# Kernel optimization log

Measured on AMD Instinct MI355X. Metric: run time of the kernel, lower is better.

## Reference

```python
import jax, jax.numpy as jnp
import numpy as np

S, T, B = 128, 64, 64          # src_len, trg_len, batch
E, H, D, A, V = 512, 512, 1024, 256, 32000  # emb, enc_hid, dec_hid(=2H), attn, vocab
PAD = 0


def _p(key, shape, scale=0.02):
    return jax.random.normal(key, shape, dtype=jnp.float32) * scale


def setup_inputs() -> dict:
    key = jax.random.key(0)
    ks = jax.random.split(key, 20)
    return {
        'src': jax.random.randint(ks[0], (S, B), 0, V, dtype=jnp.int32),
        'trg': jax.random.randint(ks[1], (T, B), 0, V, dtype=jnp.int32),
        'enc_emb': _p(ks[2], (V, E)),
        'Wf_ih': _p(ks[3], (4 * H, E)), 'Wf_hh': _p(ks[4], (4 * H, H)), 'bf': jnp.zeros((4 * H,), jnp.float32),
        'Wb_ih': _p(ks[5], (4 * H, E)), 'Wb_hh': _p(ks[6], (4 * H, H)), 'bb': jnp.zeros((4 * H,), jnp.float32),
        'Wa': _p(ks[7], (A, 2 * H + D)), 'ba': jnp.zeros((A,), jnp.float32),
        'v': _p(ks[8], (A,)),
        'dec_emb': _p(ks[9], (V, E)),
        'Wd_ih': _p(ks[10], (4 * D, E + 2 * H)), 'Wd_hh': _p(ks[11], (4 * D, D)), 'bd': jnp.zeros((4 * D,), jnp.float32),
        'Wo': _p(ks[12], (V, 2 * H + D + E)), 'bo': jnp.zeros((V,), jnp.float32),
    }


def lstm_cell(x, h, c, W_ih, W_hh, b):
    # PyTorch gate order: i, f, g, o
    g = x @ W_ih.T + h @ W_hh.T + b
    i, f, gg, o = jnp.split(g, 4, axis=-1)
    c2 = jax.nn.sigmoid(f) * c + jax.nn.sigmoid(i) * jnp.tanh(gg)
    h2 = jax.nn.sigmoid(o) * jnp.tanh(c2)
    return h2, c2


def seq2seq_fwd(src, trg, enc_emb, Wf_ih, Wf_hh, bf, Wb_ih, Wb_hh, bb,
                Wa, ba, v, dec_emb, Wd_ih, Wd_hh, bd, Wo, bo):
    emb = enc_emb[src]                                   # [S,B,E]
    z = jnp.zeros((B, H), emb.dtype)

    def fstep(carry, x):
        h, c = lstm_cell(x, *carry, Wf_ih, Wf_hh, bf)
        return (h, c), h

    def bstep(carry, x):
        h, c = lstm_cell(x, *carry, Wb_ih, Wb_hh, bb)
        return (h, c), h

    (hf, cf), hs_f = jax.lax.scan(fstep, (z, z), emb)
    (hb, cb), hs_b = jax.lax.scan(bstep, (z, z), emb[::-1])
    enc_out = jnp.concatenate([hs_f, hs_b[::-1]], axis=-1)   # [S,B,2H]

    h0 = jnp.concatenate([hf, hb], axis=-1)              # [B,D]
    c0 = jnp.concatenate([cf, cb], axis=-1)

    mask = (src != PAD).T                                # [B,S]
    enc_bse = enc_out.transpose(1, 0, 2)                 # [B,S,2H]

    def dstep(carry, tok):
        h, c = carry
        emb_t = dec_emb[tok]                             # [B,E]
        hrep = jnp.broadcast_to(h[:, None, :], (B, S, D))
        energy = jnp.tanh(jnp.concatenate([hrep, enc_bse], -1) @ Wa.T + ba)  # [B,S,A]
        scores = energy @ v                              # [B,S]
        scores = jnp.where(mask, scores, jnp.float32(-1e10))
        a = jax.nn.softmax(scores, axis=1)
        ctx = jnp.einsum('bs,bse->be', a, enc_bse)       # [B,2H]
        x = jnp.concatenate([emb_t, ctx], axis=-1)
        h2, c2 = lstm_cell(x, h, c, Wd_ih, Wd_hh, bd)
        pred = jnp.concatenate([h2, ctx, emb_t], -1) @ Wo.T + bo  # [B,V]
        return (h2, c2), pred

    # teacher_forcing_ratio = 1.0 -> input at step t is trg[t-1]
    _, preds = jax.lax.scan(dstep, (h0, c0), trg[:-1])
    outputs = jnp.concatenate([jnp.zeros((1, B, V), preds.dtype), preds], axis=0)
    return outputs                                       # [T,B,V]


def reference(src, trg, enc_emb, Wf_ih, Wf_hh, bf, Wb_ih, Wb_hh, bb,
              Wa, ba, v, dec_emb, Wd_ih, Wd_hh, bd, Wo, bo):
    return seq2seq_fwd(src, trg, enc_emb, Wf_ih, Wf_hh, bf, Wb_ih, Wb_hh, bb,
                       Wa, ba, v, dec_emb, Wd_ih, Wd_hh, bd, Wo, bo)
```

## Files before the change

kernel.cpp:

```cpp
#include <hip/hip_runtime.h>

#define SLEN  128
#define BATCH 64
#define EMB   512
#define HID   512
#define DDEC  1024
#define ATT   256
#define VOC   32000
#define TSTEPS 63
#define SLOT  1024

typedef _Float16 f16x4 __attribute__((ext_vector_type(4)));
typedef _Float16 f16x8 __attribute__((ext_vector_type(8)));
typedef float    f32x4 __attribute__((ext_vector_type(4)));

union HQ  { unsigned long long q[2]; f16x8 v; };
union HP  { _Float16 h[2]; unsigned u; };
union HP4 { _Float16 h[4]; f16x4 v4; unsigned long long u; };

__device__ __forceinline__ float sigmoidf_(float x) { return 1.0f / (1.0f + __expf(-x)); }
__device__ __forceinline__ float tanhf_(float x)    { return 1.0f - 2.0f / (__expf(2.0f * x) + 1.0f); }

__device__ __forceinline__ void st_u32(void* p, unsigned v) {
    __hip_atomic_store((unsigned*)p, v, __ATOMIC_RELAXED, __HIP_MEMORY_SCOPE_AGENT);
}
__device__ __forceinline__ void st_u64(void* p, unsigned long long v) {
    __hip_atomic_store((unsigned long long*)p, v, __ATOMIC_RELAXED, __HIP_MEMORY_SCOPE_AGENT);
}
__device__ __forceinline__ unsigned long long ld_u64(const void* p) {
    return __hip_atomic_load((const unsigned long long*)p, __ATOMIC_RELAXED, __HIP_MEMORY_SCOPE_AGENT);
}
__device__ __forceinline__ void st_i32(int* p, int v) {
    __hip_atomic_store(p, v, __ATOMIC_RELAXED, __HIP_MEMORY_SCOPE_AGENT);
}
__device__ __forceinline__ int ld_i32(const int* p) {
    return __hip_atomic_load(p, __ATOMIC_RELAXED, __HIP_MEMORY_SCOPE_AGENT);
}

__device__ __forceinline__ void barf(int* flags, int* gen, int narr, int myid,
                                     int epoch, bool amDet) {
    __syncthreads();
    if (amDet) {
        if (threadIdx.x == 0 && myid < narr) st_i32(flags + myid * SLOT, epoch);
        if ((int)threadIdx.x < narr) {
            while (ld_i32(flags + threadIdx.x * SLOT) < epoch)
                __builtin_amdgcn_s_sleep(2);
        }
        __syncthreads();
        if (threadIdx.x == 0) st_i32(gen, epoch);
    } else {
        if (threadIdx.x == 0) {
            if (myid < narr) st_i32(flags + myid * SLOT, epoch);
            while (ld_i32(gen) < epoch)
                __builtin_amdgcn_s_sleep(4);
        }
    }
    __syncthreads();
}

__global__ __launch_bounds__(256) void init_convert(
    const int* __restrict__ src, const int* __restrict__ trg,
    const float* __restrict__ enc_emb, const float* __restrict__ dec_emb,
    const float* __restrict__ Wf_ih, const float* __restrict__ Wf_hh,
    const float* __restrict__ Wb_ih, const float* __restrict__ Wb_hh,
    const float* __restrict__ Wa, const float* __restrict__ Wd_ih, const float* __restrict__ Wd_hh,
    float* __restrict__ out0,
    _Float16* __restrict__ Wenc16, _Float16* __restrict__ Wd16, _Float16* __restrict__ Wa16,
    _Float16* __restrict__ emb_src16, _Float16* __restrict__ predA,
    float* __restrict__ c_enc, _Float16* __restrict__ h16_enc, int* __restrict__ bar_ws)
{
    long idx = (long)blockIdx.x * 256 + threadIdx.x;
    if (idx < 2048000L) { out0[idx] = 0.f; return; }
    idx -= 2048000L;
    if (idx < 4194304L) {
        int dir = (int)(idx >> 21);
        int rem = (int)(idx & ((1 << 21) - 1));
        int rr = rem >> 10, c = rem & 1023;
        int d = rr >> 2, qg = rr & 3;
        const float* Wih = dir ? Wb_ih : Wf_ih;
        const float* Whh = dir ? Wb_hh : Wf_hh;
        float v = (c < 512) ? Wih[(long)(qg * 512 + d) * 512 + c]
                            : Whh[(long)(qg * 512 + d) * 512 + (c - 512)];
        Wenc16[idx] = (_Float16)v; return;
    }
    idx -= 4194304L;
    if (idx < 10485760L) {
        int rr = (int)(idx / 2560), c = (int)(idx % 2560);
        int d = rr >> 2, qg = rr & 3;
        float v = (c < 1536) ? Wd_ih[(long)(qg * 1024 + d) * 1536 + c]
                             : Wd_hh[(long)(qg * 1024 + d) * 1024 + (c - 1536)];
        Wd16[idx] = (_Float16)v; return;
    }
    idx -= 10485760L;
    if (idx < 262144L) {
        int rr = (int)(idx >> 10), c = (int)(idx & 1023);
        Wa16[idx] = (_Float16)Wa[(long)rr * 2048 + c]; return;
    }
    idx -= 262144L;
    if (idx < 4194304L) {
        int sb = (int)(idx >> 9), e = (int)(idx & 511);
        int tok = src[sb];
        emb_src16[idx] = (_Float16)enc_emb[(long)tok * 512 + e]; return;
    }
    idx -= 4194304L;
    if (idx < 2064384L) {
        int rI = (int)(idx >> 9), e = (int)(idx & 511);
        int tok = trg[rI];
        predA[(long)(64 + rI) * 2560 + 2048 + e] = (_Float16)dec_emb[(long)tok * 512 + e]; return;
    }
    idx -= 2064384L;
    if (idx < 65536L) { c_enc[idx] = 0.f; return; }
    idx -= 65536L;
    if (idx < 65536L) { h16_enc[idx] = (_Float16)0.f; return; }
    idx -= 65536L;
    if (idx < 527360L) { bar_ws[idx] = 0; }
}

__global__ __launch_bounds__(256, 1) void enc_coop(
    const _Float16* __restrict__ Wenc16, const _Float16* __restrict__ emb_src16,
    _Float16* __restrict__ h16_enc, float* __restrict__ c_enc,
    const float* __restrict__ bf, const float* __restrict__ bb,
    _Float16* __restrict__ enc_out16, int* __restrict__ bar_ws)
{
    __shared__ _Float16 Wl[16384];
    __shared__ float gbuf[16][65];

    const int t = threadIdx.x, lane = t & 63, w = t >> 6;
    const int blk = blockIdx.x, dir = blk >> 7, tile = blk & 127;
    const int r16 = lane & 15, kg = lane >> 4;
    int* gflags = bar_ws + (257 + dir * 129) * SLOT;
    int* ggen   = gflags + 128 * SLOT;
    const bool amDet = (tile == 127);

    #pragma unroll
    for (int i = 0; i < 8; ++i) {
        int h0 = (i * 256 + t) * 8;
        int kc = h0 >> 9, l = (h0 >> 3) & 63;
        f16x8 v = *(const f16x8*)(Wenc16 + ((size_t)(dir * 2048 + tile * 16 + (l & 15))) * 1024 + (l >> 4) * 8 + kc * 32);
        *(f16x8*)&Wl[h0] = v;
    }

    const float* bias = dir ? bb : bf;
    const int pb = t & 63, pp = (t >> 6) & 1;
    float bias2[2][4];
    float creg2[2] = {0.f, 0.f};
    if (t < 128) {
        #pragma unroll
        for (int j = 0; j < 2; ++j)
            #pragma unroll
            for (int q = 0; q < 4; ++q)
                bias2[j][q] = bias[q * 512 + tile * 4 + pp * 2 + j];
    }
    __syncthreads();

    for (int s = 0; s < SLEN; ++s) {
        const int par = s & 1;
        const int s_eff = dir ? (127 - s) : s;
        const _Float16* Ax = emb_src16 + ((size_t)(s_eff * 64 + w * 16 + r16)) * 512 + kg * 8;
        const unsigned long long* Hq =
            (const unsigned long long*)(h16_enc + ((size_t)((par * 2 + dir) * 64 + w * 16 + r16)) * 512);
        f32x4 a0 = {}, a1 = {};
        #pragma unroll 8
        for (int kc = 0; kc < 16; ++kc) {
            f16x8 bx = *(const f16x8*)&Wl[kc * 512 + lane * 8];
            f16x8 ax = *(const f16x8*)(Ax + kc * 32);
            a0 = __builtin_amdgcn_mfma_f32_16x16x32_f16(ax, bx, a0, 0, 0, 0);
            f16x8 bh = *(const f16x8*)&Wl[(16 + kc) * 512 + lane * 8];
            HQ hq;
            hq.q[0] = ld_u64(Hq + kc * 8 + kg * 2);
            hq.q[1] = ld_u64(Hq + kc * 8 + kg * 2 + 1);
            a1 = __builtin_amdgcn_mfma_f32_16x16x32_f16(hq.v, bh, a1, 0, 0, 0);
        }
        #pragma unroll
        for (int rI = 0; rI < 4; ++rI)
            gbuf[r16][w * 16 + kg * 4 + rI] = a0[rI] + a1[rI];
        __syncthreads();
        if (t < 128) {
            HP hp;
            #pragma unroll
            for (int j = 0; j < 2; ++j) {
                const int dl = pp * 2 + j;
                float g0 = gbuf[dl * 4 + 0][pb] + bias2[j][0];
                float g1 = gbuf[dl * 4 + 1][pb] + bias2[j][1];
                float g2 = gbuf[dl * 4 + 2][pb] + bias2[j][2];
                float g3 = gbuf[dl * 4 + 3][pb] + bias2[j][3];
                float c2 = sigmoidf_(g1) * creg2[j] + sigmoidf_(g0) * tanhf_(g2);
                float h2 = sigmoidf_(g3) * tanhf_(c2);
                creg2[j] = c2;
                hp.h[j] = (_Float16)h2;
            }
            const int d0 = tile * 4 + pp * 2;
            st_u32((void*)(h16_enc + ((size_t)((par ^ 1) * 2 + dir) * 64 + pb) * 512 + d0), hp.u);
            *(unsigned*)(enc_out16 + ((size_t)s_eff * 64 + pb) * 1024 + dir * 512 + d0) = hp.u;
        }
        barf(gflags, ggen, 128, tile, s + 1, amDet);
    }
    if (t < 128) {
        const int d0 = tile * 4 + pp * 2;
        c_enc[((size_t)dir * 64 + pb) * 512 + d0] = creg2[0];
        c_enc[((size_t)dir * 64 + pb) * 512 + d0 + 1] = creg2[1];
    }
}

__global__ __launch_bounds__(256, 1) void dec_coop(
    const _Float16* __restrict__ Wd16, const _Float16* __restrict__ Wa16,
    const float* __restrict__ bd, const float* __restrict__ vvec,
    const int* __restrict__ src, const _Float16* __restrict__ enc_part16,
    const _Float16* __restrict__ enc_out16, const float* __restrict__ c_enc,
    _Float16* __restrict__ predA, int* __restrict__ bar_ws)
{
    __shared__ _Float16 Wl[40960];
    __shared__ float gbuf[16][65];
    __shared__ float ha[256], sv[256], sc[128], red[128];

    const int t = threadIdx.x, lane = t & 63, w = t >> 6;
    const int tile = blockIdx.x;
    const int r16 = lane & 15, kg = lane >> 4;
    int* gflags = bar_ws;
    int* ggen   = gflags + 256 * SLOT;
    const bool amDet = (tile == 255);

    #pragma unroll
    for (int i = 0; i < 20; ++i) {
        int h0 = (i * 256 + t) * 8;
        int kc = h0 >> 9, l = (h0 >> 3) & 63;
        f16x8 v = *(const f16x8*)(Wd16 + ((size_t)(tile * 16 + (l & 15))) * 2560 + (l >> 4) * 8 + kc * 32);
        *(f16x8*)&Wl[h0] = v;
    }

    const int pb = t & 63, pp = (t >> 6) & 1;
    float bias2[2][4], creg2[2] = {0.f, 0.f};
    if (t < 128) {
        #pragma unroll
        for (int j = 0; j < 2; ++j) {
            const int dg = tile * 4 + pp * 2 + j;
            #pragma unroll
            for (int q = 0; q < 4; ++q) bias2[j][q] = bd[q * 1024 + dg];
            creg2[j] = (dg < 512) ? c_enc[(size_t)pb * 512 + dg]
                                  : c_enc[(size_t)(64 + pb) * 512 + (dg - 512)];
        }
    }

    const int b0 = blockIdx.x;
    if (b0 < 64) {
        sv[t] = vvec[t];
        #pragma unroll
        for (int i = 0; i < 2; ++i) {
            int pidx = i * 256 + t;
            int d = pidx * 2;
            const size_t rbase = (d < 512) ? (size_t)(127 * 64 + b0) * 1024 : (size_t)(0 * 64 + b0) * 1024;
            HP hp;
            hp.h[0] = enc_out16[rbase + d];
            hp.h[1] = enc_out16[rbase + d + 1];
            st_u32((void*)(predA + (size_t)b0 * 2560 + d), hp.u);
        }
    }
    barf(gflags, ggen, 64, tile, 1, amDet);

    for (int tt = 0; tt < TSTEPS; ++tt) {
        if (b0 < 64) {
            const int base_m = b0 & 48;
            const _Float16* Ahh = predA + ((size_t)(tt * 64 + base_m + r16)) * 2560 + kg * 8;
            f32x4 acc4[4] = {};
            #pragma unroll 4
            for (int kc = 0; kc < 32; ++kc) {
                f16x8 a = *(const f16x8*)(Ahh + kc * 32);
                #pragma unroll
                for (int jj = 0; jj < 4; ++jj) {
                    f16x8 bw = *(const f16x8*)(Wa16 + ((size_t)((w * 4 + jj) * 16 + r16)) * 1024 + kg * 8 + kc * 32);
                    acc4[jj] = __builtin_amdgcn_mfma_f32_16x16x32_f16(a, bw, acc4[jj], 0, 0, 0);
                }
            }
            if (kg == ((b0 & 15) >> 2)) {
                #pragma unroll
                for (int jj = 0; jj < 4; ++jj)
                    ha[(w * 4 + jj) * 16 + r16] = acc4[jj][b0 & 3];
            }
            __syncthreads();
            if (t < 128) {
                const f16x8* ep = (const f16x8*)(enc_part16 + ((size_t)t * 64 + b0) * 256);
                float acc = 0.f;
                #pragma unroll 4
                for (int j8 = 0; j8 < 32; ++j8) {
                    f16x8 e = ep[j8];
                    #pragma unroll
                    for (int u = 0; u < 8; ++u)
                        acc += tanhf_(ha[j8 * 8 + u] + (float)e[u]) * sv[j8 * 8 + u];
                }
                float scv = (src[t * 64 + b0] != 0) ? acc : -1e10f;
                sc[t] = scv; red[t] = scv;
            }
            __syncthreads();
            for (int off = 64; off > 0; off >>= 1) { if (t < off) red[t] = fmaxf(red[t], red[t + off]); __syncthreads(); }
            const float mx = red[0];
            __syncthreads();
            if (t < 128) { float e = __expf(sc[t] - mx); sc[t] = e; red[t] = e; }
            __syncthreads();
            for (int off = 64; off > 0; off >>= 1) { if (t < off) red[t] += red[t + off]; __syncthreads(); }
            const float inv = 1.0f / red[0];
            __syncthreads();
            float a0 = 0.f, a1 = 0.f, a2 = 0.f, a3 = 0.f;
            for (int sI = 0; sI < 128; ++sI) {
                float as = sc[sI] * inv;
                f16x4 ev = *(const f16x4*)(enc_out16 + ((size_t)sI * 64 + b0) * 1024 + t * 4);
                a0 += as * (float)ev[0]; a1 += as * (float)ev[1];
                a2 += as * (float)ev[2]; a3 += as * (float)ev[3];
            }
            HP4 o;
            o.h[0] = (_Float16)a0; o.h[1] = (_Float16)a1;
            o.h[2] = (_Float16)a2; o.h[3] = (_Float16)a3;
            st_u64((void*)(predA + ((size_t)(64 + tt * 64 + b0)) * 2560 + 1024 + t * 4), o.u);
        }
        barf(gflags, ggen, 64, tile, 2 * tt + 2, amDet);
        {
            const _Float16* Ae = predA + ((size_t)(64 + tt * 64 + w * 16 + r16)) * 2560 + kg * 8;
            const _Float16* Ah = predA + ((size_t)(tt * 64 + w * 16 + r16)) * 2560 + kg * 8;
            f32x4 ae = {}, ac = {}, ah = {};
            #pragma unroll 8
            for (int kc = 0; kc < 16; ++kc) {
                f16x8 bw = *(const f16x8*)&Wl[kc * 512 + lane * 8];
                f16x8 a = *(const f16x8*)(Ae + 2048 + kc * 32);
                ae = __builtin_amdgcn_mfma_f32_16x16x32_f16(a, bw, ae, 0, 0, 0);
            }
            #pragma unroll 8
            for (int kc = 0; kc < 32; ++kc) {
                f16x8 bw = *(const f16x8*)&Wl[(16 + kc) * 512 + lane * 8];
                f16x8 a = *(const f16x8*)(Ae + 1024 + kc * 32);
                ac = __builtin_amdgcn_mfma_f32_16x16x32_f16(a, bw, ac, 0, 0, 0);
            }
            #pragma unroll 8
            for (int kc = 0; kc < 32; ++kc) {
                f16x8 bw = *(const f16x8*)&Wl[(48 + kc) * 512 + lane * 8];
                f16x8 a = *(const f16x8*)(Ah + kc * 32);
                ah = __builtin_amdgcn_mfma_f32_16x16x32_f16(a, bw, ah, 0, 0, 0);
            }
            #pragma unroll
            for (int rI = 0; rI < 4; ++rI)
                gbuf[r16][w * 16 + kg * 4 + rI] = ae[rI] + ac[rI] + ah[rI];
            __syncthreads();
            if (t < 128) {
                HP hp;
                #pragma unroll
                for (int j = 0; j < 2; ++j) {
                    const int dl = pp * 2 + j;
                    float g0 = gbuf[dl * 4 + 0][pb] + bias2[j][0];
                    float g1 = gbuf[dl * 4 + 1][pb] + bias2[j][1];
                    float g2 = gbuf[dl * 4 + 2][pb] + bias2[j][2];
                    float g3 = gbuf[dl * 4 + 3][pb] + bias2[j][3];
                    float c2 = sigmoidf_(g1) * creg2[j] + sigmoidf_(g0) * tanhf_(g2);
                    float h2 = sigmoidf_(g3) * tanhf_(c2);
                    creg2[j] = c2;
                    hp.h[j] = (_Float16)h2;
                }
                st_u32((void*)(predA + ((size_t)(64 + tt * 64 + pb)) * 2560 + tile * 4 + pp * 2), hp.u);
            }
        }
        barf(gflags, ggen, 256, tile, 2 * tt + 3, amDet);
    }
}

__global__ __launch_bounds__(64) void enc_step_mfma(
    const _Float16* __restrict__ Wenc16, const _Float16* __restrict__ emb_src16,
    _Float16* __restrict__ h16_enc, float* __restrict__ c_enc,
    const float* __restrict__ bf, const float* __restrict__ bb,
    _Float16* __restrict__ enc_out16, int s)
{
    __shared__ float gbuf[16 * 66];
    const int lane = threadIdx.x;
    const int blk = blockIdx.x;
    const int dir = blk >> 7, tile = blk & 127;
    const int par = s & 1;
    const int s_eff = dir ? (SLEN - 1 - s) : s;
    const int r16 = lane & 15, kg = lane >> 4;

    const _Float16* Bw = Wenc16 + ((size_t)(dir * 2048 + tile * 16 + r16)) * 1024 + kg * 8;
    const _Float16* Ax = emb_src16 + ((size_t)(s_eff * 64 + r16)) * 512 + kg * 8;
    const _Float16* Ah = h16_enc + ((size_t)((par * 2 + dir) * 64 + r16)) * 512 + kg * 8;

    f32x4 acc[4] = {};
    #pragma unroll 4
    for (int kc = 0; kc < 16; ++kc) {
        f16x8 bfr = *(const f16x8*)(Bw + kc * 32);
        #pragma unroll
        for (int m = 0; m < 4; ++m) {
            f16x8 a = *(const f16x8*)(Ax + kc * 32 + (size_t)m * 16 * 512);
            acc[m] = __builtin_amdgcn_mfma_f32_16x16x32_f16(a, bfr, acc[m], 0, 0, 0);
        }
    }
    #pragma unroll 4
    for (int kc = 0; kc < 16; ++kc) {
        f16x8 bfr = *(const f16x8*)(Bw + 512 + kc * 32);
        #pragma unroll
        for (int m = 0; m < 4; ++m) {
            f16x8 a = *(const f16x8*)(Ah + kc * 32 + (size_t)m * 16 * 512);
            acc[m] = __builtin_amdgcn_mfma_f32_16x16x32_f16(a, bfr, acc[m], 0, 0, 0);
        }
    }
    #pragma unroll
    for (int m = 0; m < 4; ++m)
        #pragma unroll
        for (int rI = 0; rI < 4; ++rI)
            gbuf[r16 * 66 + m * 16 + kg * 4 + rI] = acc[m][rI];
    __syncthreads();

    const float* bias = dir ? bb : bf;
    const int b = lane;
    #pragma unroll
    for (int dl = 0; dl < 4; ++dl) {
        const int d = tile * 4 + dl;
        float g0 = gbuf[(dl * 4 + 0) * 66 + b] + bias[d];
        float g1 = gbuf[(dl * 4 + 1) * 66 + b] + bias[512 + d];
        float g2 = gbuf[(dl * 4 + 2) * 66 + b] + bias[1024 + d];
        float g3 = gbuf[(dl * 4 + 3) * 66 + b] + bias[1536 + d];
        const size_t cur = ((size_t)(par * 2 + dir) * 64 + b) * 512 + d;
        const size_t nxt = ((size_t)((par ^ 1) * 2 + dir) * 64 + b) * 512 + d;
        float c2 = sigmoidf_(g1) * c_enc[cur] + sigmoidf_(g0) * tanhf_(g2);
        float h2 = sigmoidf_(g3) * tanhf_(c2);
        c_enc[nxt] = c2;
        h16_enc[nxt] = (_Float16)h2;
        enc_out16[((size_t)s_eff * 64 + b) * 1024 + dir * 512 + d] = (_Float16)h2;
    }
}

__global__ __launch_bounds__(256) void dec_init(
    const _Float16* __restrict__ enc_out16, const float* __restrict__ c_enc,
    _Float16* __restrict__ predA, float* __restrict__ c_dec)
{
    int idx = blockIdx.x * 256 + threadIdx.x;
    int b = (idx >> 10) & 63, d = idx & 1023;
    if (idx < 65536) {
        _Float16 v = (d < 512) ? enc_out16[(size_t)(127 * 64 + b) * 1024 + d]
                               : enc_out16[(size_t)(0 * 64 + b) * 1024 + d];
        predA[(size_t)b * 2560 + d] = v;
    } else {
        float v = (d < 512) ? c_enc[((size_t)(0 * 2 + 0) * 64 + b) * 512 + d]
                            : c_enc[((size_t)(0 * 2 + 1) * 64 + b) * 512 + (d - 512)];
        c_dec[(size_t)b * 1024 + d] = v;
    }
}

__global__ __launch_bounds__(64) void hatt_mfma(
    const _Float16* __restrict__ predA, const _Float16* __restrict__ Wa16,
    float* __restrict__ hatt, int t)
{
    const int lane = threadIdx.x;
    const int tile = blockIdx.x;
    const int r16 = lane & 15, kg = lane >> 4;
    const _Float16* Ap = predA + ((size_t)(t * 64 + r16)) * 2560 + kg * 8;
    const _Float16* Bw = Wa16 + ((size_t)(tile * 16 + r16)) * 1024 + kg * 8;
    f32x4 acc[4] = {};
    #pragma unroll 4
    for (int kc = 0; kc < 32; ++kc) {
        f16x8 bfr = *(const f16x8*)(Bw + kc * 32);
        #pragma unroll
        for (int m = 0; m < 4; ++m) {
            f16x8 a = *(const f16x8*)(Ap + kc * 32 + (size_t)m * 16 * 2560);
            acc[m] = __builtin_amdgcn_mfma_f32_16x16x32_f16(a, bfr, acc[m], 0, 0, 0);
        }
    }
    #pragma unroll
    for (int m = 0; m < 4; ++m)
        #pragma unroll
        for (int rI = 0; rI < 4; ++rI)
            hatt[(size_t)(m * 16 + kg * 4 + rI) * 256 + tile * 16 + r16] = acc[m][rI];
}

__global__ __launch_bounds__(256) void attn_step(
    const int* __restrict__ src, const float* __restrict__ hatt, const float* __restrict__ vvec,
    const _Float16* __restrict__ enc_part16, const _Float16* __restrict__ enc_out16,
    _Float16* __restrict__ predA, int t)
{
    __shared__ float ha[256], sv[256], sc[128], red[128];
    const int b = blockIdx.x, tid = threadIdx.x;
    ha[tid] = hatt[b * 256 + tid];
    sv[tid] = vvec[tid];
    __syncthreads();
    if (tid < 128) {
        const f16x8* ep = (const f16x8*)(enc_part16 + ((size_t)tid * 64 + b) * 256);
        float acc = 0.f;
        #pragma unroll 4
        for (int j8 = 0; j8 < 32; ++j8) {
            f16x8 e = ep[j8];
            #pragma unroll
            for (int u = 0; u < 8; ++u)
                acc += tanhf_(ha[j8 * 8 + u] + (float)e[u]) * sv[j8 * 8 + u];
        }
        float scv = (src[tid * 64 + b] != 0) ? acc : -1e10f;
        sc[tid] = scv; red[tid] = scv;
    }
    __syncthreads();
    for (int off = 64; off > 0; off >>= 1) { if (tid < off) red[tid] = fmaxf(red[tid], red[tid + off]); __syncthreads(); }
    const float mx = red[0];
    __syncthreads();
    if (tid < 128) { float e = __expf(sc[tid] - mx); sc[tid] = e; red[tid] = e; }
    __syncthreads();
    for (int off = 64; off > 0; off >>= 1) { if (tid < off) red[tid] += red[tid + off]; __syncthreads(); }
    const float inv = 1.0f / red[0];
    __syncthreads();

    float a0 = 0.f, a1 = 0.f, a2 = 0.f, a3 = 0.f;
    for (int sI = 0; sI < 128; ++sI) {
        float as = sc[sI] * inv;
        f16x4 ev = *(const f16x4*)(enc_out16 + ((size_t)sI * 64 + b) * 1024 + tid * 4);
        a0 += as * (float)ev[0]; a1 += as * (float)ev[1];
        a2 += as * (float)ev[2]; a3 += as * (float)ev[3];
    }
    f16x4 o = { (_Float16)a0, (_Float16)a1, (_Float16)a2, (_Float16)a3 };
    *(f16x4*)(predA + ((size_t)(64 + t * 64 + b)) * 2560 + 1024 + tid * 4) = o;
}

__global__ __launch_bounds__(64) void dec_gates(
    const _Float16* __restrict__ Wd16, const float* __restrict__ bd,
    float* __restrict__ c_dec, _Float16* __restrict__ predA, int t)
{
    __shared__ float gbuf[16 * 66];
    const int lane = threadIdx.x;
    const int tile = blockIdx.x;
    const int par = t & 1;
    const int r16 = lane & 15, kg = lane >> 4;
    const _Float16* Bw = Wd16 + ((size_t)(tile * 16 + r16)) * 2560 + kg * 8;
    const _Float16* At = predA + ((size_t)(64 + t * 64 + r16)) * 2560 + kg * 8;
    const _Float16* Ah = predA + ((size_t)(t * 64 + r16)) * 2560 + kg * 8;
    f32x4 acc[4] = {};
    #pragma unroll 4
    for (int kc = 0; kc < 16; ++kc) {
        f16x8 bfr = *(const f16x8*)(Bw + kc * 32);
        #pragma unroll
        for (int m = 0; m < 4; ++m) {
            f16x8 a = *(const f16x8*)(At + 2048 + kc * 32 + (size_t)m * 16 * 2560);
            acc[m] = __builtin_amdgcn_mfma_f32_16x16x32_f16(a, bfr, acc[m], 0, 0, 0);
        }
    }
    #pragma unroll 4
    for (int kc = 0; kc < 32; ++kc) {
        f16x8 bfr = *(const f16x8*)(Bw + 512 + kc * 32);
        #pragma unroll
        for (int m = 0; m < 4; ++m) {
            f16x8 a = *(const f16x8*)(At + 1024 + kc * 32 + (size_t)m * 16 * 2560);
            acc[m] = __builtin_amdgcn_mfma_f32_16x16x32_f16(a, bfr, acc[m], 0, 0, 0);
        }
    }
    #pragma unroll 4
    for (int kc = 0; kc < 32; ++kc) {
        f16x8 bfr = *(const f16x8*)(Bw + 1536 + kc * 32);
        #pragma unroll
        for (int m = 0; m < 4; ++m) {
            f16x8 a = *(const f16x8*)(Ah + kc * 32 + (size_t)m * 16 * 2560);
            acc[m] = __builtin_amdgcn_mfma_f32_16x16x32_f16(a, bfr, acc[m], 0, 0, 0);
        }
    }
    #pragma unroll
    for (int m = 0; m < 4; ++m)
        #pragma unroll
        for (int rI = 0; rI < 4; ++rI)
            gbuf[r16 * 66 + m * 16 + kg * 4 + rI] = acc[m][rI];
    __syncthreads();

    const int b = lane;
    #pragma unroll
    for (int dl = 0; dl < 4; ++dl) {
        const int d = tile * 4 + dl;
        float g0 = gbuf[(dl * 4 + 0) * 66 + b] + bd[d];
        float g1 = gbuf[(dl * 4 + 1) * 66 + b] + bd[1024 + d];
        float g2 = gbuf[(dl * 4 + 2) * 66 + b] + bd[2048 + d];
        float g3 = gbuf[(dl * 4 + 3) * 66 + b] + bd[3072 + d];
        float c2 = sigmoidf_(g1) * c_dec[(size_t)(par * 64 + b) * 1024 + d] + sigmoidf_(g0) * tanhf_(g2);
        float h2 = sigmoidf_(g3) * tanhf_(c2);
        c_dec[(size_t)((par ^ 1) * 64 + b) * 1024 + d] = c2;
        predA[((size_t)(64 + t * 64 + b)) * 2560 + d] = (_Float16)h2;
    }
}

__global__ __launch_bounds__(256, 2) void gemm_a16(
    const _Float16* __restrict__ A, int lda,
    const float* __restrict__ B, int ldb,
    const float* __restrict__ bias,
    void* __restrict__ Cv, int ldc, int K, int Mvalid, int ntn, int c16)
{
    __shared__ _Float16 As[8192];
    __shared__ _Float16 Bs[8192];

    const int nwg = gridDim.x;
    const int id = blockIdx.x;
    const int q = nwg >> 3, r = nwg & 7;
    const int xcd = id & 7, ix = id >> 3;
    const int wg = (xcd < r) ? (xcd * (q + 1) + ix) : (r * (q + 1) + (xcd - r) * q + ix);
    const int per = ntn << 3;
    const int g = wg / per, rem = wg % per;
    const int mt = g * 8 + (rem & 7), nt = rem >> 3;

    const int t = threadIdx.x, lane = t & 63, wid = t >> 6;
    const int wr = wid >> 1, wc = wid & 1;

    const int arow_s = t >> 3, ac8 = t & 7;
    const int brow_s = t >> 4, bc4 = t & 15;
    const _Float16* Ap = A + (size_t)(mt * 128 + arow_s) * lda + ac8 * 8;
    const float*    Bp = B + (size_t)(nt * 128 + brow_s) * ldb + bc4 * 4;
    const int awx = (ac8 * 8) ^ ((arow_s & 7) << 3);
    const int bwx = (bc4 * 4) ^ ((brow_s & 7) << 3);

    const int kts = K >> 6;
    f32x4 acc[4][4] = {};
    f16x8 ra[4]; float4 rb[8];
    #pragma unroll
    for (int i = 0; i < 4; ++i) ra[i] = *(const f16x8*)(Ap + (size_t)i * 32 * lda);
    #pragma unroll
    for (int i = 0; i < 8; ++i) rb[i] = *(const float4*)(Bp + (size_t)i * 16 * ldb);

    const int abase = (wr * 64 + (lane & 15)) * 64 + (lane >> 4) * 8;
    const int bbase = (wc * 64 + (lane & 15)) * 64 + (lane >> 4) * 8;
    const int sxor = (lane & 7) << 3;

    for (int kt = 0; kt < kts; ++kt) {
        f16x4 cb[8];
        #pragma unroll
        for (int i = 0; i < 8; ++i)
            cb[i] = (f16x4){(_Float16)rb[i].x, (_Float16)rb[i].y, (_Float16)rb[i].z, (_Float16)rb[i].w};
        __syncthreads();
        #pragma unroll
        for (int i = 0; i < 4; ++i)
            *(f16x8*)&As[(arow_s + i * 32) * 64 + awx] = ra[i];
        #pragma unroll
        for (int i = 0; i < 8; ++i)
            *(f16x4*)&Bs[(brow_s + i * 16) * 64 + bwx] = cb[i];
        __syncthreads();
        if (kt + 1 < kts) {
            #pragma unroll
            for (int i = 0; i < 4; ++i) ra[i] = *(const f16x8*)(Ap + (size_t)i * 32 * lda + (kt + 1) * 64);
            #pragma unroll
            for (int i = 0; i < 8; ++i) rb[i] = *(const float4*)(Bp + (size_t)i * 16 * ldb + (kt + 1) * 64);
        }
        #pragma unroll
        for (int kk = 0; kk < 2; ++kk) {
            f16x8 af[4], bfr[4];
            #pragma unroll
            for (int m = 0; m < 4; ++m) af[m]  = *(const f16x8*)&As[(abase + m * 16 * 64 + kk * 32) ^ sxor];
            #pragma unroll
            for (int n = 0; n < 4; ++n) bfr[n] = *(const f16x8*)&Bs[(bbase + n * 16 * 64 + kk * 32) ^ sxor];
            #pragma unroll
            for (int m = 0; m < 4; ++m)
                #pragma unroll
                for (int n = 0; n < 4; ++n)
                    acc[m][n] = __builtin_amdgcn_mfma_f32_16x16x32_f16(af[m], bfr[n], acc[m][n], 0, 0, 0);
        }
    }

    const int ccol = nt * 128 + wc * 64 + (lane & 15);
    const int crow0 = mt * 128 + wr * 64 + ((lane >> 4) << 2);
    float bv[4];
    #pragma unroll
    for (int n = 0; n < 4; ++n) bv[n] = bias[ccol + n * 16];
    #pragma unroll
    for (int m = 0; m < 4; ++m) {
        #pragma unroll
        for (int rI = 0; rI < 4; ++rI) {
            const int row = crow0 + m * 16 + rI;
            if (row < Mvalid) {
                if (c16) {
                    _Float16* C = (_Float16*)Cv;
                    #pragma unroll
                    for (int n = 0; n < 4; ++n)
                        C[(size_t)row * ldc + ccol + n * 16] = (_Float16)(acc[m][n][rI] + bv[n]);
                } else {
                    float* C = (float*)Cv;
                    #pragma unroll
                    for (int n = 0; n < 4; ++n)
                        C[(size_t)row * ldc + ccol + n * 16] = acc[m][n][rI] + bv[n];
                }
            }
        }
    }
}

extern "C" void kernel_launch(void* const* d_in, const int* in_sizes, int n_in,
                              void* d_out, int out_size, void* d_ws, size_t ws_size,
                              hipStream_t stream) {
    const int*   src     = (const int*)d_in[0];
    const int*   trg     = (const int*)d_in[1];
    const float* enc_emb = (const float*)d_in[2];
    const float* Wf_ih   = (const float*)d_in[3];
    const float* Wf_hh   = (const float*)d_in[4];
    const float* bf      = (const float*)d_in[5];
    const float* Wb_ih   = (const float*)d_in[6];
    const float* Wb_hh   = (const float*)d_in[7];
    const float* bb      = (const float*)d_in[8];
    const float* Wa      = (const float*)d_in[9];
    const float* ba      = (const float*)d_in[10];
    const float* vvec    = (const float*)d_in[11];
    const float* dec_emb = (const float*)d_in[12];
    const float* Wd_ih   = (const float*)d_in[13];
    const float* Wd_hh   = (const float*)d_in[14];
    const float* bd      = (const float*)d_in[15];
    const float* Wo      = (const float*)d_in[16];
    const float* bo      = (const float*)d_in[17];
    float* out = (float*)d_out;

    char* w = (char*)d_ws;
    _Float16* Wenc16     = (_Float16*)(w);
    _Float16* Wd16       = (_Float16*)(w + 8388608);
    _Float16* Wa16       = (_Float16*)(w + 29360128);
    _Float16* emb_src16  = (_Float16*)(w + 29884416);
    _Float16* enc_out16  = (_Float16*)(w + 38273024);
    _Float16* predA      = (_Float16*)(w + 55050240);
    _Float16* h16_enc    = (_Float16*)(w + 76349440);
    float*    c_enc      = (float*)   (w + 76611584);
    float*    c_dec      = (float*)   (w + 77135872);
    float*    hatt       = (float*)   (w + 77660160);
    _Float16* enc_part16 = (_Float16*)(w + 77725696);
    int*      bar_ws     = (int*)     (w + 81920000);
    const size_t need_bytes = 84029440;
    if (ws_size < need_bytes) return;

    init_convert<<<93428, 256, 0, stream>>>(
        src, trg, enc_emb, dec_emb, Wf_ih, Wf_hh, Wb_ih, Wb_hh, Wa, Wd_ih, Wd_hh,
        out, Wenc16, Wd16, Wa16, emb_src16, predA, c_enc, h16_enc, bar_ws);

    {
        const _Float16* a0 = Wenc16; const _Float16* a1 = emb_src16;
        _Float16* a2 = h16_enc; float* a3 = c_enc;
        const float* a4 = bf; const float* a5 = bb;
        _Float16* a6 = enc_out16; int* a7 = bar_ws;
        void* args[] = { &a0, &a1, &a2, &a3, &a4, &a5, &a6, &a7 };
        hipError_t e = hipLaunchCooperativeKernel((const void*)enc_coop, dim3(256), dim3(256), args, 0, stream);
        if (e != hipSuccess) {
            for (int s = 0; s < SLEN; ++s)
                enc_step_mfma<<<256, 64, 0, stream>>>(Wenc16, emb_src16, h16_enc, c_enc, bf, bb, enc_out16, s);
        }
    }

    gemm_a16<<<128, 256, 0, stream>>>(enc_out16, 1024, Wa + 1024, 2048, ba,
                                      enc_part16, 256, 1024, 8192, 2, 1);

    {
        const _Float16* a0 = Wd16; const _Float16* a1 = Wa16;
        const float* a2 = bd; const float* a3 = vvec;
        const int* a4 = src; const _Float16* a5 = enc_part16;
        const _Float16* a6 = enc_out16; const float* a7 = c_enc;
        _Float16* a8 = predA; int* a9 = bar_ws;
        void* args[] = { &a0, &a1, &a2, &a3, &a4, &a5, &a6, &a7, &a8, &a9 };
        hipError_t e = hipLaunchCooperativeKernel((const void*)dec_coop, dim3(256), dim3(256), args, 0, stream);
        if (e != hipSuccess) {
            dec_init<<<512, 256, 0, stream>>>(enc_out16, c_enc, predA, c_dec);
            for (int t = 0; t < TSTEPS; ++t) {
                hatt_mfma<<<16, 64, 0, stream>>>(predA, Wa16, hatt, t);
                attn_step<<<64, 256, 0, stream>>>(src, hatt, vvec, enc_part16, enc_out16, predA, t);
                dec_gates<<<256, 64, 0, stream>>>(Wd16, bd, c_dec, predA, t);
            }
        }
    }

    gemm_a16<<<8000, 256, 0, stream>>>(predA + (size_t)64 * 2560, 2560, Wo, 2560, bo,
                                       out + (size_t)64 * VOC, VOC, 2560, 4032, 250, 0);
}
```

Measured before the change: 5.999 ms.

## Repartition encoder and decoder cooperative kernels across fewer blocks with LDS-staged activations

The encoder now splits work into four groups (direction × batch half) of 64 blocks, each handling 32 hidden units for 32 batch rows. It stages the input embedding and hidden state in swizzled LDS and holds a larger weight tile in LDS. The decoder drops from 256 to 64 blocks of 512 threads, so every block computes attention and the gate GEMM while streaming Wd from global memory instead of LDS. Grid barriers now span only 64 participants, which reduces sync cost, but each block carries more per-step work and the decoder loses its LDS-resident weights.

Result: slower. 6.867 ms (+14.5%).

```diff
diff --git a/kernel.cpp b/kernel.cpp
--- a/kernel.cpp
+++ b/kernel.cpp
@@ -113,7 +113,7 @@
     idx -= 65536L;
     if (idx < 65536L) { h16_enc[idx] = (_Float16)0.f; return; }
     idx -= 65536L;
-    if (idx < 527360L) { bar_ws[idx] = 0; }
+    if (idx < 332800L) { bar_ws[idx] = 0; }
 }
 
 __global__ __launch_bounds__(256, 1) void enc_coop(
@@ -122,64 +122,85 @@
     const float* __restrict__ bf, const float* __restrict__ bb,
     _Float16* __restrict__ enc_out16, int* __restrict__ bar_ws)
 {
-    __shared__ _Float16 Wl[16384];
-    __shared__ float gbuf[16][65];
-
-    const int t = threadIdx.x, lane = t & 63, w = t >> 6;
-    const int blk = blockIdx.x, dir = blk >> 7, tile = blk & 127;
+    __shared__ _Float16 Wl[32768];
+    __shared__ _Float16 Xs[32 * 1024];
+    __shared__ float gbuf[32][34];
+
+    const int t = threadIdx.x, lane = t & 63, wv = t >> 6;
+    const int blk = blockIdx.x;
+    const int g = blk >> 6, wb = blk & 63;
+    const int dir = g >> 1, bh = g & 1;
     const int r16 = lane & 15, kg = lane >> 4;
-    int* gflags = bar_ws + (257 + dir * 129) * SLOT;
-    int* ggen   = gflags + 128 * SLOT;
-    const bool amDet = (tile == 127);
-
-    #pragma unroll
-    for (int i = 0; i < 8; ++i) {
+    int* gflags = bar_ws + (65 + g * 65) * SLOT;
+    int* ggen   = gflags + 64 * SLOT;
+    const bool amDet = (wb == 63);
+
+    #pragma unroll
+    for (int i = 0; i < 16; ++i) {
         int h0 = (i * 256 + t) * 8;
-        int kc = h0 >> 9, l = (h0 >> 3) & 63;
-        f16x8 v = *(const f16x8*)(Wenc16 + ((size_t)(dir * 2048 + tile * 16 + (l & 15))) * 1024 + (l >> 4) * 8 + kc * 32);
+        int kc = h0 >> 10;
+        int rem = h0 & 1023;
+        int gt = rem >> 9, l = (rem >> 3) & 63;
+        f16x8 v = *(const f16x8*)(Wenc16 +
+            ((size_t)(dir * 2048 + wb * 32 + gt * 16 + (l & 15))) * 1024 + (l >> 4) * 8 + kc * 32);
         *(f16x8*)&Wl[h0] = v;
     }
 
     const float* bias = dir ? bb : bf;
-    const int pb = t & 63, pp = (t >> 6) & 1;
-    float bias2[2][4];
-    float creg2[2] = {0.f, 0.f};
+    const int pb = t & 31, dp = t >> 5;
+    const int dl0 = dp * 2;
+    float bias2[2][4], creg2[2] = {0.f, 0.f};
     if (t < 128) {
         #pragma unroll
         for (int j = 0; j < 2; ++j)
             #pragma unroll
             for (int q = 0; q < 4; ++q)
-                bias2[j][q] = bias[q * 512 + tile * 4 + pp * 2 + j];
+                bias2[j][q] = bias[q * 512 + wb * 8 + dl0 + j];
     }
     __syncthreads();
 
     for (int s = 0; s < SLEN; ++s) {
         const int par = s & 1;
         const int s_eff = dir ? (127 - s) : s;
-        const _Float16* Ax = emb_src16 + ((size_t)(s_eff * 64 + w * 16 + r16)) * 512 + kg * 8;
-        const unsigned long long* Hq =
-            (const unsigned long long*)(h16_enc + ((size_t)((par * 2 + dir) * 64 + w * 16 + r16)) * 512);
-        f32x4 a0 = {}, a1 = {};
-        #pragma unroll 8
-        for (int kc = 0; kc < 16; ++kc) {
-            f16x8 bx = *(const f16x8*)&Wl[kc * 512 + lane * 8];
-            f16x8 ax = *(const f16x8*)(Ax + kc * 32);
-            a0 = __builtin_amdgcn_mfma_f32_16x16x32_f16(ax, bx, a0, 0, 0, 0);
-            f16x8 bh = *(const f16x8*)&Wl[(16 + kc) * 512 + lane * 8];
-            HQ hq;
-            hq.q[0] = ld_u64(Hq + kc * 8 + kg * 2);
-            hq.q[1] = ld_u64(Hq + kc * 8 + kg * 2 + 1);
-            a1 = __builtin_amdgcn_mfma_f32_16x16x32_f16(hq.v, bh, a1, 0, 0, 0);
-        }
-        #pragma unroll
-        for (int rI = 0; rI < 4; ++rI)
-            gbuf[r16][w * 16 + kg * 4 + rI] = a0[rI] + a1[rI];
+        #pragma unroll
+        for (int i = 0; i < 8; ++i) {
+            int slot = i * 256 + t;
+            int row = slot >> 6, c8 = slot & 63;
+            f16x8 v = *(const f16x8*)(emb_src16 +
+                ((size_t)(s_eff * 64 + bh * 32 + row)) * 512 + c8 * 8);
+            *(f16x8*)((char*)Xs + row * 2048 + ((c8 * 16) ^ ((row & 7) << 4))) = v;
+        }
+        #pragma unroll
+        for (int i = 0; i < 8; ++i) {
+            int slot = i * 256 + t;
+            int row = slot >> 6, c8 = slot & 63;
+            const unsigned long long* hp = (const unsigned long long*)(h16_enc +
+                ((size_t)((par * 2 + dir) * 64 + bh * 32 + row)) * 512 + c8 * 8);
+            HQ hq; hq.q[0] = ld_u64(hp); hq.q[1] = ld_u64(hp + 1);
+            *(f16x8*)((char*)Xs + row * 2048 + (((64 + c8) * 16) ^ ((row & 7) << 4))) = hq.v;
+        }
+        __syncthreads();
+        {
+            const int gt = wv & 1, mb = wv >> 1;
+            const int arow = mb * 16 + r16;
+            f32x4 acc = {};
+            #pragma unroll 8
+            for (int kc = 0; kc < 32; ++kc) {
+                f16x8 bw = *(const f16x8*)&Wl[kc * 1024 + gt * 512 + lane * 8];
+                f16x8 a = *(const f16x8*)((char*)Xs + arow * 2048 +
+                           ((kg * 16 + kc * 64) ^ ((arow & 7) << 4)));
+                acc = __builtin_amdgcn_mfma_f32_16x16x32_f16(a, bw, acc, 0, 0, 0);
+            }
+            #pragma unroll
+            for (int rI = 0; rI < 4; ++rI)
+                gbuf[gt * 16 + (lane & 15)][mb * 16 + kg * 4 + rI] = acc[rI];
+        }
         __syncthreads();
         if (t < 128) {
             HP hp;
             #pragma unroll
             for (int j = 0; j < 2; ++j) {
-                const int dl = pp * 2 + j;
+                const int dl = dl0 + j;
                 float g0 = gbuf[dl * 4 + 0][pb] + bias2[j][0];
                 float g1 = gbuf[dl * 4 + 1][pb] + bias2[j][1];
                 float g2 = gbuf[dl * 4 + 2][pb] + bias2[j][2];
@@ -189,77 +210,66 @@
                 creg2[j] = c2;
                 hp.h[j] = (_Float16)h2;
             }
-            const int d0 = tile * 4 + pp * 2;
-            st_u32((void*)(h16_enc + ((size_t)((par ^ 1) * 2 + dir) * 64 + pb) * 512 + d0), hp.u);
-            *(unsigned*)(enc_out16 + ((size_t)s_eff * 64 + pb) * 1024 + dir * 512 + d0) = hp.u;
-        }
-        barf(gflags, ggen, 128, tile, s + 1, amDet);
+            const int bglob = bh * 32 + pb;
+            const int d0 = wb * 8 + dl0;
+            st_u32((void*)(h16_enc + ((size_t)((par ^ 1) * 2 + dir) * 64 + bglob) * 512 + d0), hp.u);
+            *(unsigned*)(enc_out16 + ((size_t)s_eff * 64 + bglob) * 1024 + dir * 512 + d0) = hp.u;
+        }
+        barf(gflags, ggen, 64, wb, s + 1, amDet);
     }
     if (t < 128) {
-        const int d0 = tile * 4 + pp * 2;
-        c_enc[((size_t)dir * 64 + pb) * 512 + d0] = creg2[0];
-        c_enc[((size_t)dir * 64 + pb) * 512 + d0 + 1] = creg2[1];
-    }
-}
-
-__global__ __launch_bounds__(256, 1) void dec_coop(
+        const int bglob = bh * 32 + pb;
+        const int d0 = wb * 8 + dl0;
+        c_enc[((size_t)dir * 64 + bglob) * 512 + d0] = creg2[0];
+        c_enc[((size_t)dir * 64 + bglob) * 512 + d0 + 1] = creg2[1];
+    }
+}
+
+__global__ __launch_bounds__(512, 1) void dec_coop(
     const _Float16* __restrict__ Wd16, const _Float16* __restrict__ Wa16,
     const float* __restrict__ bd, const float* __restrict__ vvec,
     const int* __restrict__ src, const _Float16* __restrict__ enc_part16,
     const _Float16* __restrict__ enc_out16, const float* __restrict__ c_enc,
     _Float16* __restrict__ predA, int* __restrict__ bar_ws)
 {
-    __shared__ _Float16 Wl[40960];
-    __shared__ float gbuf[16][65];
+    __shared__ _Float16 Xs[64 * 512];
+    __shared__ float gbuf[64][66];
     __shared__ float ha[256], sv[256], sc[128], red[128];
 
-    const int t = threadIdx.x, lane = t & 63, w = t >> 6;
-    const int tile = blockIdx.x;
+    const int t = threadIdx.x, lane = t & 63, wv = t >> 6;
+    const int wb = blockIdx.x;
     const int r16 = lane & 15, kg = lane >> 4;
     int* gflags = bar_ws;
-    int* ggen   = gflags + 256 * SLOT;
-    const bool amDet = (tile == 255);
-
-    #pragma unroll
-    for (int i = 0; i < 20; ++i) {
-        int h0 = (i * 256 + t) * 8;
-        int kc = h0 >> 9, l = (h0 >> 3) & 63;
-        f16x8 v = *(const f16x8*)(Wd16 + ((size_t)(tile * 16 + (l & 15))) * 2560 + (l >> 4) * 8 + kc * 32);
-        *(f16x8*)&Wl[h0] = v;
-    }
-
-    const int pb = t & 63, pp = (t >> 6) & 1;
-    float bias2[2][4], creg2[2] = {0.f, 0.f};
-    if (t < 128) {
-        #pragma unroll
-        for (int j = 0; j < 2; ++j) {
-            const int dg = tile * 4 + pp * 2 + j;
-            #pragma unroll
-            for (int q = 0; q < 4; ++q) bias2[j][q] = bd[q * 1024 + dg];
-            creg2[j] = (dg < 512) ? c_enc[(size_t)pb * 512 + dg]
-                                  : c_enc[(size_t)(64 + pb) * 512 + (dg - 512)];
-        }
-    }
-
-    const int b0 = blockIdx.x;
-    if (b0 < 64) {
-        sv[t] = vvec[t];
-        #pragma unroll
-        for (int i = 0; i < 2; ++i) {
-            int pidx = i * 256 + t;
-            int d = pidx * 2;
-            const size_t rbase = (d < 512) ? (size_t)(127 * 64 + b0) * 1024 : (size_t)(0 * 64 + b0) * 1024;
-            HP hp;
-            hp.h[0] = enc_out16[rbase + d];
-            hp.h[1] = enc_out16[rbase + d + 1];
-            st_u32((void*)(predA + (size_t)b0 * 2560 + d), hp.u);
-        }
-    }
-    barf(gflags, ggen, 64, tile, 1, amDet);
+    int* ggen   = gflags + 64 * SLOT;
+    const bool amDet = (wb == 63);
+
+    const int pb = t & 63;
+    const int dl0 = (t >> 6) * 2;
+    float bias2[2][4], creg2[2];
+    #pragma unroll
+    for (int j = 0; j < 2; ++j) {
+        const int dg = wb * 16 + dl0 + j;
+        #pragma unroll
+        for (int q = 0; q < 4; ++q) bias2[j][q] = bd[q * 1024 + dg];
+        creg2[j] = (dg < 512) ? c_enc[(size_t)pb * 512 + dg]
+                              : c_enc[(size_t)(64 + pb) * 512 + (dg - 512)];
+    }
+    if (t < 256) sv[t] = vvec[t];
+
+    {
+        int d = t * 2;
+        const size_t rbase = (d < 512) ? (size_t)(127 * 64 + wb) * 1024
+                                       : (size_t)(0 * 64 + wb) * 1024;
+        HP hp;
+        hp.h[0] = enc_out16[rbase + d];
+        hp.h[1] = enc_out16[rbase + d + 1];
+        st_u32((void*)(predA + (size_t)wb * 2560 + d), hp.u);
+    }
+    barf(gflags, ggen, 64, wb, 1, amDet);
 
     for (int tt = 0; tt < TSTEPS; ++tt) {
-        if (b0 < 64) {
-            const int base_m = b0 & 48;
+        if (t < 256) {
+            const int base_m = wb & 48;
             const _Float16* Ahh = predA + ((size_t)(tt * 64 + base_m + r16)) * 2560 + kg * 8;
             f32x4 acc4[4] = {};
             #pragma unroll 4
@@ -267,95 +277,113 @@
                 f16x8 a = *(const f16x8*)(Ahh + kc * 32);
                 #pragma unroll
                 for (int jj = 0; jj < 4; ++jj) {
-                    f16x8 bw = *(const f16x8*)(Wa16 + ((size_t)((w * 4 + jj) * 16 + r16)) * 1024 + kg * 8 + kc * 32);
+                    f16x8 bw = *(const f16x8*)(Wa16 +
+                        ((size_t)((wv * 4 + jj) * 16 + r16)) * 1024 + kg * 8 + kc * 32);
                     acc4[jj] = __builtin_amdgcn_mfma_f32_16x16x32_f16(a, bw, acc4[jj], 0, 0, 0);
                 }
             }
-            if (kg == ((b0 & 15) >> 2)) {
+            if (kg == ((wb & 15) >> 2)) {
                 #pragma unroll
                 for (int jj = 0; jj < 4; ++jj)
-                    ha[(w * 4 + jj) * 16 + r16] = acc4[jj][b0 & 3];
-            }
-            __syncthreads();
-            if (t < 128) {
-                const f16x8* ep = (const f16x8*)(enc_part16 + ((size_t)t * 64 + b0) * 256);
-                float acc = 0.f;
-                #pragma unroll 4
-                for (int j8 = 0; j8 < 32; ++j8) {
-                    f16x8 e = ep[j8];
-                    #pragma unroll
-                    for (int u = 0; u < 8; ++u)
-                        acc += tanhf_(ha[j8 * 8 + u] + (float)e[u]) * sv[j8 * 8 + u];
-                }
-                float scv = (src[t * 64 + b0] != 0) ? acc : -1e10f;
-                sc[t] = scv; red[t] = scv;
-            }
-            __syncthreads();
-            for (int off = 64; off > 0; off >>= 1) { if (t < off) red[t] = fmaxf(red[t], red[t + off]); __syncthreads(); }
-            const float mx = red[0];
-            __syncthreads();
-            if (t < 128) { float e = __expf(sc[t] - mx); sc[t] = e; red[t] = e; }
-            __syncthreads();
-            for (int off = 64; off > 0; off >>= 1) { if (t < off) red[t] += red[t + off]; __syncthreads(); }
-            const float inv = 1.0f / red[0];
-            __syncthreads();
+                    ha[(wv * 4 + jj) * 16 + r16] = acc4[jj][wb & 3];
+            }
+        }
+        __syncthreads();
+        if (t < 128) {
+            const f16x8* ep = (const f16x8*)(enc_part16 + ((size_t)t * 64 + wb) * 256);
+            float acc = 0.f;
+            #pragma unroll 4
+            for (int j8 = 0; j8 < 32; ++j8) {
+                f16x8 e = ep[j8];
+                #pragma unroll
+                for (int u = 0; u < 8; ++u)
+                    acc += tanhf_(ha[j8 * 8 + u] + (float)e[u]) * sv[j8 * 8 + u];
+            }
+            float scv = (src[t * 64 + wb] != 0) ? acc : -1e10f;
+            sc[t] = scv; red[t] = scv;
+        }
+        __syncthreads();
+        for (int off = 64; off > 0; off >>= 1) { if (t < off) red[t] = fmaxf(red[t], red[t + off]); __syncthreads(); }
+        const float mx = red[0];
+        __syncthreads();
+        if (t < 128) { float e = __expf(sc[t] - mx); sc[t] = e; red[t] = e; }
+        __syncthreads();
+        for (int off = 64; off > 0; off >>= 1) { if (t < off) red[t] += red[t + off]; __syncthreads(); }
+        const float inv = 1.0f / red[0];
+        __syncthreads();
+        if (t < 256) {
             float a0 = 0.f, a1 = 0.f, a2 = 0.f, a3 = 0.f;
             for (int sI = 0; sI < 128; ++sI) {
                 float as = sc[sI] * inv;
-                f16x4 ev = *(const f16x4*)(enc_out16 + ((size_t)sI * 64 + b0) * 1024 + t * 4);
+                f16x4 ev = *(const f16x4*)(enc_out16 + ((size_t)sI * 64 + wb) * 1024 + t * 4);
                 a0 += as * (float)ev[0]; a1 += as * (float)ev[1];
                 a2 += as * (float)ev[2]; a3 += as * (float)ev[3];
             }
             HP4 o;
             o.h[0] = (_Float16)a0; o.h[1] = (_Float16)a1;
             o.h[2] = (_Float16)a2; o.h[3] = (_Float16)a3;
-            st_u64((void*)(predA + ((size_t)(64 + tt * 64 + b0)) * 2560 + 1024 + t * 4), o.u);
-        }
-        barf(gflags, ggen, 64, tile, 2 * tt + 2, amDet);
+            st_u64((void*)(predA + ((size_t)(64 + tt * 64 + wb)) * 2560 + 1024 + t * 4), o.u);
+        }
+        barf(gflags, ggen, 64, wb, 2 * tt + 2, amDet);
+
         {
-            const _Float16* Ae = predA + ((size_t)(64 + tt * 64 + w * 16 + r16)) * 2560 + kg * 8;
-            const _Float16* Ah = predA + ((size_t)(tt * 64 + w * 16 + r16)) * 2560 + kg * 8;
-            f32x4 ae = {}, ac = {}, ah = {};
-            #pragma unroll 8
-            for (int kc = 0; kc < 16; ++kc) {
-                f16x8 bw = *(const f16x8*)&Wl[kc * 512 + lane * 8];
-                f16x8 a = *(const f16x8*)(Ae + 2048 + kc * 32);
-                ae = __builtin_amdgcn_mfma_f32_16x16x32_f16(a, bw, ae, 0, 0, 0);
-            }
-            #pragma unroll 8
-            for (int kc = 0; kc < 32; ++kc) {
-                f16x8 bw = *(const f16x8*)&Wl[(16 + kc) * 512 + lane * 8];
-                f16x8 a = *(const f16x8*)(Ae + 1024 + kc * 32);
-                ac = __builtin_amdgcn_mfma_f32_16x16x32_f16(a, bw, ac, 0, 0, 0);
-            }
-            #pragma unroll 8
-            for (int kc = 0; kc < 32; ++kc) {
-                f16x8 bw = *(const f16x8*)&Wl[(48 + kc) * 512 + lane * 8];
-                f16x8 a = *(const f16x8*)(Ah + kc * 32);
-                ah = __builtin_amdgcn_mfma_f32_16x16x32_f16(a, bw, ah, 0, 0, 0);
-            }
-            #pragma unroll
-            for (int rI = 0; rI < 4; ++rI)
-                gbuf[r16][w * 16 + kg * 4 + rI] = ae[rI] + ac[rI] + ah[rI];
-            __syncthreads();
-            if (t < 128) {
-                HP hp;
+            const int gt = wv & 3;
+            const int bh = wv >> 2;
+            f32x4 acc2[2] = {};
+            #pragma unroll
+            for (int c = 0; c < 5; ++c) {
+                int rb, cb;
+                if      (c == 0) { rb = 64 + tt * 64; cb = 2048; }
+                else if (c == 1) { rb = 64 + tt * 64; cb = 1024; }
+                else if (c == 2) { rb = 64 + tt * 64; cb = 1536; }
+                else if (c == 3) { rb = tt * 64;      cb = 0;    }
+                else             { rb = tt * 64;      cb = 512;  }
+                __syncthreads();
                 #pragma unroll
-                for (int j = 0; j < 2; ++j) {
-                    const int dl = pp * 2 + j;
-                    float g0 = gbuf[dl * 4 + 0][pb] + bias2[j][0];
-                    float g1 = gbuf[dl * 4 + 1][pb] + bias2[j][1];
-                    float g2 = gbuf[dl * 4 + 2][pb] + bias2[j][2];
-                    float g3 = gbuf[dl * 4 + 3][pb] + bias2[j][3];
-                    float c2 = sigmoidf_(g1) * creg2[j] + sigmoidf_(g0) * tanhf_(g2);
-                    float h2 = sigmoidf_(g3) * tanhf_(c2);
-                    creg2[j] = c2;
-                    hp.h[j] = (_Float16)h2;
+                for (int i = 0; i < 8; ++i) {
+                    int slot = i * 512 + t;
+                    int row = slot >> 6, c8 = slot & 63;
+                    f16x8 v = *(const f16x8*)(predA + (size_t)(rb + row) * 2560 + cb + c8 * 8);
+                    *(f16x8*)((char*)Xs + row * 1024 + ((c8 * 16) ^ ((row & 7) << 4))) = v;
                 }
-                st_u32((void*)(predA + ((size_t)(64 + tt * 64 + pb)) * 2560 + tile * 4 + pp * 2), hp.u);
-            }
-        }
-        barf(gflags, ggen, 256, tile, 2 * tt + 3, amDet);
+                __syncthreads();
+                const _Float16* Bp = Wd16 + (size_t)(wb * 64 + gt * 16 + r16) * 2560 + c * 512 + kg * 8;
+                #pragma unroll 4
+                for (int kcL = 0; kcL < 16; ++kcL) {
+                    f16x8 bw = *(const f16x8*)(Bp + kcL * 32);
+                    #pragma unroll
+                    for (int m = 0; m < 2; ++m) {
+                        const int arow = bh * 32 + m * 16 + r16;
+                        f16x8 a = *(const f16x8*)((char*)Xs + arow * 1024 +
+                                   ((kg * 16 + kcL * 64) ^ ((arow & 7) << 4)));
+                        acc2[m] = __builtin_amdgcn_mfma_f32_16x16x32_f16(a, bw, acc2[m], 0, 0, 0);
+                    }
+                }
+            }
+            #pragma unroll
+            for (int m = 0; m < 2; ++m)
+                #pragma unroll
+                for (int rI = 0; rI < 4; ++rI)
+                    gbuf[gt * 16 + (lane & 15)][bh * 32 + m * 16 + kg * 4 + rI] = acc2[m][rI];
+        }
+        __syncthreads();
+        {
+            HP hp;
+            #pragma unroll
+            for (int j = 0; j < 2; ++j) {
+                const int dl = dl0 + j;
+                float g0 = gbuf[dl * 4 + 0][pb] + bias2[j][0];
+                float g1 = gbuf[dl * 4 + 1][pb] + bias2[j][1];
+                float g2 = gbuf[dl * 4 + 2][pb] + bias2[j][2];
+                float g3 = gbuf[dl * 4 + 3][pb] + bias2[j][3];
+                float c2 = sigmoidf_(g1) * creg2[j] + sigmoidf_(g0) * tanhf_(g2);
+                float h2 = sigmoidf_(g3) * tanhf_(c2);
+                creg2[j] = c2;
+                hp.h[j] = (_Float16)h2;
+            }
+            st_u32((void*)(predA + ((size_t)(64 + tt * 64 + pb)) * 2560 + wb * 16 + dl0), hp.u);
+        }
+        barf(gflags, ggen, 64, wb, 2 * tt + 3, amDet);
     }
 }
 
@@ -708,10 +736,10 @@
     float*    hatt       = (float*)   (w + 77660160);
     _Float16* enc_part16 = (_Float16*)(w + 77725696);
     int*      bar_ws     = (int*)     (w + 81920000);
-    const size_t need_bytes = 84029440;
+    const size_t need_bytes = 83251200;
     if (ws_size < need_bytes) return;
 
-    init_convert<<<93428, 256, 0, stream>>>(
+    init_convert<<<92628, 256, 0, stream>>>(
         src, trg, enc_emb, dec_emb, Wf_ih, Wf_hh, Wb_ih, Wb_hh, Wa, Wd_ih, Wd_hh,
         out, Wenc16, Wd16, Wa16, emb_src16, predA, c_enc, h16_enc, bar_ws);
 
@@ -738,7 +766,7 @@
         const _Float16* a6 = enc_out16; const float* a7 = c_enc;
         _Float16* a8 = predA; int* a9 = bar_ws;
         void* args[] = { &a0, &a1, &a2, &a3, &a4, &a5, &a6, &a7, &a8, &a9 };
-        hipError_t e = hipLaunchCooperativeKernel((const void*)dec_coop, dim3(256), dim3(256), args, 0, stream);
+        hipError_t e = hipLaunchCooperativeKernel((const void*)dec_coop, dim3(64), dim3(512), args, 0, stream);
         if (e != hipSuccess) {
             dec_init<<<512, 256, 0, stream>>>(enc_out16, c_enc, predA, c_dec);
             for (int t = 0; t < TSTEPS; ++t) {
```
